# Kernel optimization log

Hardware: AMD Instinct MI355X
Metric: run time of the kernel (lower is better)

## Reference

```python
import jax, jax.numpy as jnp
import numpy as np


def _lstm_last(x, wih, whh, bih, bhh):
    """PyTorch-semantics LSTM over x [B, T, I]; returns last hidden state [B, H].
    Gate order in weights: i, f, g, o (PyTorch convention)."""
    B = x.shape[0]
    H = whh.shape[1]
    b = bih + bhh

    def step(carry, xt):
        h, c = carry
        g = xt @ wih.T + h @ whh.T + b  # [B, 4H]
        i, f, gg, o = jnp.split(g, 4, axis=-1)
        c = jax.nn.sigmoid(f) * c + jax.nn.sigmoid(i) * jnp.tanh(gg)
        h = jax.nn.sigmoid(o) * jnp.tanh(c)
        return (h, c), None

    h0 = jnp.zeros((B, H), x.dtype)
    (h, _), _ = jax.lax.scan(step, (h0, h0), jnp.swapaxes(x, 0, 1))
    return h


def setup_inputs() -> dict:
    key = jax.random.key(0)
    ks = jax.random.split(key, 16)
    B, N, T = 512, 32, 50
    s = 0.05
    return {
        "agent_traj": jax.random.normal(ks[0], (B, T, 2), jnp.float32),
        "neighbour_traj": jax.random.normal(ks[1], (B, N, T, 2), jnp.float32),
        "a_wih": jax.random.normal(ks[2], (256, 2), jnp.float32) * s,
        "a_whh": jax.random.normal(ks[3], (256, 64), jnp.float32) * s,
        "a_bih": jax.random.normal(ks[4], (256,), jnp.float32) * s,
        "a_bhh": jax.random.normal(ks[5], (256,), jnp.float32) * s,
        "n_wih": jax.random.normal(ks[6], (256, 2), jnp.float32) * s,
        "n_whh": jax.random.normal(ks[7], (256, 64), jnp.float32) * s,
        "n_bih": jax.random.normal(ks[8], (256,), jnp.float32) * s,
        "n_bhh": jax.random.normal(ks[9], (256,), jnp.float32) * s,
        "d_wih": jax.random.normal(ks[10], (512, 128), jnp.float32) * s,
        "d_whh": jax.random.normal(ks[11], (512, 128), jnp.float32) * s,
        "d_bih": jax.random.normal(ks[12], (512,), jnp.float32) * s,
        "d_bhh": jax.random.normal(ks[13], (512,), jnp.float32) * s,
        "e_w": jax.random.normal(ks[14], (2, 128), jnp.float32) * s,
        "e_b": jax.random.normal(ks[15], (2,), jnp.float32) * s,
    }


def reference(agent_traj, neighbour_traj, a_wih, a_whh, a_bih, a_bhh,
              n_wih, n_whh, n_bih, n_bhh, d_wih, d_whh, d_bih, d_bhh, e_w, e_b):
    B, N, T, _ = neighbour_traj.shape
    # agent encoder: last hidden state [B, 64]
    agent_emb = _lstm_last(agent_traj, a_wih, a_whh, a_bih, a_bhh)
    # neighbour encoder: batch all B*N ragged sequences as one LSTM call, then mean over neighbours
    nh = _lstm_last(neighbour_traj.reshape(B * N, T, 2), n_wih, n_whh, n_bih, n_bhh)
    neigh_emb = nh.reshape(B, N, 64).mean(axis=1)  # [B, 64]

    h0 = jnp.concatenate([agent_emb, neigh_emb], axis=1)  # [B, 128]
    c0 = jnp.zeros_like(h0)
    db = d_bih + d_bhh

    def dec_step(carry, _):
        h, c = carry
        # LSTMCell with input = h itself
        g = h @ d_wih.T + h @ d_whh.T + db  # [B, 512]
        i, f, gg, o = jnp.split(g, 4, axis=-1)
        c = jax.nn.sigmoid(f) * c + jax.nn.sigmoid(i) * jnp.tanh(gg)
        h = jax.nn.sigmoid(o) * jnp.tanh(c)
        pred = h @ e_w.T + e_b  # [B, 2]
        return (h, c), pred

    _, preds = jax.lax.scan(dec_step, (h0, c0), None, length=30)  # [30, B, 2]
    return jnp.swapaxes(preds, 0, 1)  # [B, 30, 2]
```

## Files before the change

### kernel.cpp

```cpp
#include <hip/hip_runtime.h>
#include <hip/hip_bf16.h>


typedef __attribute__((ext_vector_type(8))) short bf16x8;
typedef __attribute__((ext_vector_type(4))) float f32x4;
typedef unsigned int uint;
typedef unsigned short ushort_t;

#define LOG2E  1.4426950408889634f
#define LOG2E2 2.8853900817779268f

__device__ __forceinline__ float rcp_fast(float x) { return __builtin_amdgcn_rcpf(x); }
__device__ __forceinline__ float exp2_fast(float x) { return __builtin_amdgcn_exp2f(x); }
__device__ __forceinline__ float sigf(float x) { return rcp_fast(1.0f + __expf(-x)); }
__device__ __forceinline__ float tanh_fast(float x) {
    x = fminf(fmaxf(x, -15.0f), 15.0f);
    float e = __expf(2.0f * x);
    return (e - 1.0f) * rcp_fast(e + 1.0f);
}
__device__ __forceinline__ ushort_t bf_hi(float f) {
    union { float f; uint u; } v; v.f = f;
    return (ushort_t)(v.u >> 16);
}
__device__ __forceinline__ ushort_t bf_rtn(float f) {
    union { float f; uint u; } v; v.f = f;
    return (ushort_t)((v.u + 0x7FFFu + ((v.u >> 16) & 1u)) >> 16);
}
__device__ __forceinline__ float bf_f(ushort_t h) {
    union { float f; uint u; } v; v.u = ((uint)h) << 16;
    return v.f;
}

__device__ __forceinline__ float cell_update_p(float xi, float xf, float xg,
                                               float xo, float& c) {
    float pi = exp2_fast(-xi);
    float pf = exp2_fast(-xf);
    float po = exp2_fast(-xo);
    float pg = exp2_fast(fminf(xg, 120.0f));
    float f  = rcp_fast(1.0f + pf);
    float ig = (pg - 1.0f) * rcp_fast((1.0f + pi) * (pg + 1.0f));
    float cc = __builtin_fmaf(f, c, ig);
    c = cc;
    float e2 = exp2_fast(fminf(cc * LOG2E2, 120.0f));
    return (e2 - 1.0f) * rcp_fast((1.0f + po) * (e2 + 1.0f));
}

#define HS 36

__global__ __launch_bounds__(256, 4) void enc10_kernel(
    const float* __restrict__ ax, const float* __restrict__ nx,
    const float* __restrict__ a_wih, const float* __restrict__ a_whh,
    const float* __restrict__ a_bih, const float* __restrict__ a_bhh,
    const float* __restrict__ n_wih, const float* __restrict__ n_whh,
    const float* __restrict__ n_bih, const float* __restrict__ n_bhh,
    float* __restrict__ nh_out, float* __restrict__ ah_out)
{
    const int tid = threadIdx.x, blk = blockIdx.x;
    const bool agent = (blk >= 1024);
    const int seq0 = (agent ? (blk - 1024) : blk) * 16;
    const float* __restrict__ x   = agent ? ax : nx;
    const float* __restrict__ wih = agent ? a_wih : n_wih;
    const float* __restrict__ whh = agent ? a_whh : n_whh;
    const float* __restrict__ bih = agent ? a_bih : n_bih;
    const float* __restrict__ bhh = agent ? a_bhh : n_bhh;
    float* __restrict__ hout = agent ? ah_out : nh_out;

    const int lane = tid & 63, wv = tid >> 6;
    const int col = lane & 15, quad = lane >> 4;

    __shared__ __attribute__((aligned(16))) uint hb[2][16][HS];
    __shared__ __attribute__((aligned(16))) ushort_t xb[50][16][8];

    bf16x8 Aw[4][2];
    #pragma unroll
    for (int g = 0; g < 4; ++g) {
        const float sc = (g == 2) ? LOG2E2 : LOG2E;
        #pragma unroll
        for (int kt = 0; kt < 2; ++kt) {
            const float* p = whh + (size_t)(g * 64 + 16 * wv + col) * 64 + kt * 32 + quad * 8;
            float4 v0 = *(const float4*)p;
            float4 v1 = *(const float4*)(p + 4);
            float vv[8] = { v0.x, v0.y, v0.z, v0.w, v1.x, v1.y, v1.z, v1.w };
            bf16x8 h8;
            #pragma unroll
            for (int j = 0; j < 8; ++j) h8[j] = (short)bf_rtn(vv[j] * sc);
            Aw[g][kt] = h8;
        }
    }

    bf16x8 Ax[4];
    #pragma unroll
    for (int g = 0; g < 4; ++g) {
        const float sc = (g == 2) ? LOG2E2 : LOG2E;
        bf16x8 a;
        #pragma unroll
        for (int j = 0; j < 8; ++j) a[j] = 0;
        if (quad == 0) {
            const int row = g * 64 + 16 * wv + col;
            float w0 = wih[2 * row] * sc, w1 = wih[2 * row + 1] * sc;
            float b  = (bih[row] + bhh[row]) * sc;
            ushort_t w0h = bf_hi(w0), w1h = bf_hi(w1);
            ushort_t bh  = bf_hi(b);
            a[0] = (short)w0h;
            a[1] = (short)w1h;
            a[2] = (short)bf_hi(w0 - bf_f(w0h));
            a[3] = (short)bf_hi(w1 - bf_f(w1h));
            a[4] = (short)w0h;
            a[5] = (short)w1h;
            a[6] = (short)bh;
            a[7] = (short)bf_hi(b - bf_f(bh));
        }
        Ax[g] = a;
    }

    for (int idx = tid; idx < 50 * 16; idx += 256) {
        const int t = idx >> 4, s = idx & 15;
        const float* xp = x + (size_t)(seq0 + s) * 100 + 2 * t;
        float x0 = xp[0], x1 = xp[1];
        ushort_t h0 = bf_hi(x0), h1 = bf_hi(x1);
        ushort_t* e = &xb[t][s][0];
        e[0] = h0; e[1] = h1;
        e[2] = h0; e[3] = h1;
        e[4] = bf_hi(x0 - bf_f(h0));
        e[5] = bf_hi(x1 - bf_f(h1));
        e[6] = 0x3F80; e[7] = 0x3F80;
    }
    for (int i = tid; i < 16 * HS; i += 256) (&hb[0][0][0])[i] = 0u;
    __syncthreads();

    float c[4] = {0.f, 0.f, 0.f, 0.f};
    bf16x8 Bx = *(const bf16x8*)&xb[0][col][0];

    for (int t = 0; t < 50; ++t) {
        const int cur = t & 1, nxt = cur ^ 1;

        const f32x4 z4 = {0.f, 0.f, 0.f, 0.f};
        f32x4 acc[4];
        #pragma unroll
        for (int g = 0; g < 4; ++g)
            acc[g] = __builtin_amdgcn_mfma_f32_16x16x32_bf16(Ax[g], Bx, z4, 0, 0, 0);

        #pragma unroll
        for (int kt = 0; kt < 2; ++kt) {
            bf16x8 Bhi = *(const bf16x8*)&hb[cur][col][kt * 16 + quad * 4];
            #pragma unroll
            for (int g = 0; g < 4; ++g)
                acc[g] = __builtin_amdgcn_mfma_f32_16x16x32_bf16(Aw[g][kt], Bhi, acc[g], 0, 0, 0);
        }

        float hv[4];
        #pragma unroll
        for (int r = 0; r < 4; ++r)
            hv[r] = cell_update_p(acc[0][r], acc[1][r], acc[2][r], acc[3][r], c[r]);

        {
            __hip_bfloat162 p01 = __float22bfloat162_rn(make_float2(hv[0], hv[1]));
            __hip_bfloat162 p23 = __float22bfloat162_rn(make_float2(hv[2], hv[3]));
            uint2 hi2;
            union { __hip_bfloat162 b; uint u; } c0, c1;
            c0.b = p01; c1.b = p23;
            hi2.x = c0.u;
            hi2.y = c1.u;
            const int di = 8 * wv + 2 * quad;
            *(uint2*)&hb[nxt][col][di] = hi2;
        }
        if (t < 49) Bx = *(const bf16x8*)&xb[t + 1][col][0];
        if (t == 49) {
            #pragma unroll
            for (int r = 0; r < 4; ++r)
                hout[(size_t)(seq0 + col) * 64 + 16 * wv + 4 * quad + r] = hv[r];
        }
        __syncthreads();
    }
}

__global__ __launch_bounds__(512) void dec10_kernel(
    const float* __restrict__ ah, const float* __restrict__ nh,
    const float* __restrict__ d_wih, const float* __restrict__ d_whh,
    const float* __restrict__ d_bih, const float* __restrict__ d_bhh,
    const float* __restrict__ e_w, const float* __restrict__ e_b,
    float* __restrict__ out)
{
    const int tid = threadIdx.x;
    const int blk = blockIdx.x;

    const int u  = tid >> 2;
    const int tt = tid & 3;
    const int r  = tt * 128 + u;

    float w[128];
    #pragma unroll
    for (int k = 0; k < 128; k += 4) {
        float4 aa = *(const float4*)(d_wih + r * 128 + k);
        float4 bb = *(const float4*)(d_whh + r * 128 + k);
        w[k]   = aa.x + bb.x;
        w[k+1] = aa.y + bb.y;
        w[k+2] = aa.z + bb.z;
        w[k+3] = aa.w + bb.w;
    }
    const float bias = d_bih[r] + d_bhh[r];

    __shared__ float hs[2][128];
    __shared__ float cs[2][128];
    __shared__ float gs[2][512];
    __shared__ float ews[2][128];
    __shared__ float ebs[2];

    if (tid < 256) {
        const int s = tid >> 7, j = tid & 127;
        const int gseq = blk * 2 + s;
        float v;
        if (j < 64) {
            v = ah[(size_t)gseq * 64 + j];
        } else {
            float acc = 0.0f;
            for (int n = 0; n < 32; ++n)
                acc += nh[(size_t)(gseq * 32 + n) * 64 + (j - 64)];
            v = acc * (1.0f / 32.0f);
        }
        hs[s][j] = v;
        cs[s][j] = 0.0f;
        ews[s][j] = e_w[tid];
    }
    if (tid < 2) ebs[tid] = e_b[tid];
    __syncthreads();

    for (int t = 0; t < 30; ++t) {
        #pragma unroll
        for (int s = 0; s < 2; ++s) {
            const float4* hp = (const float4*)(&hs[s][0]);
            float a0 = 0.f, a1 = 0.f, a2 = 0.f, a3 = 0.f;
            #pragma unroll
            for (int k = 0; k < 32; ++k) {
                float4 h4 = hp[k];
                a0 = __builtin_fmaf(w[4*k+0], h4.x, a0);
                a1 = __builtin_fmaf(w[4*k+1], h4.y, a1);
                a2 = __builtin_fmaf(w[4*k+2], h4.z, a2);
                a3 = __builtin_fmaf(w[4*k+3], h4.w, a3);
            }
            gs[s][tid] = bias + ((a0 + a1) + (a2 + a3));
        }
        __syncthreads();
        if (tid < 256) {
            const int s = tid >> 7, j = tid & 127;
            float4 g4 = *(const float4*)(&gs[s][4 * j]);
            float ig = sigf(g4.x), fg = sigf(g4.y);
            float gg = tanh_fast(g4.z), og = sigf(g4.w);
            float c = fg * cs[s][j] + ig * gg;
            cs[s][j] = c;
            hs[s][j] = og * tanh_fast(c);
        }
        __syncthreads();
        {
            const int wv = tid >> 6, l = tid & 63;
            if (wv < 4) {
                const int s = wv >> 1, o = wv & 1;
                float p = hs[s][l] * ews[o][l] + hs[s][64 + l] * ews[o][64 + l];
                #pragma unroll
                for (int off = 32; off > 0; off >>= 1) p += __shfl_down(p, off);
                if (l == 0) out[((size_t)(blk * 2 + s) * 30 + t) * 2 + o] = p + ebs[o];
            }
        }
    }
}

extern "C" void kernel_launch(void* const* d_in, const int* in_sizes, int n_in,
                              void* d_out, int out_size, void* d_ws, size_t ws_size,
                              hipStream_t stream)
{
    const float* agent_traj = (const float*)d_in[0];
    const float* neigh_traj = (const float*)d_in[1];
    const float* a_wih = (const float*)d_in[2];
    const float* a_whh = (const float*)d_in[3];
    const float* a_bih = (const float*)d_in[4];
    const float* a_bhh = (const float*)d_in[5];
    const float* n_wih = (const float*)d_in[6];
    const float* n_whh = (const float*)d_in[7];
    const float* n_bih = (const float*)d_in[8];
    const float* n_bhh = (const float*)d_in[9];
    const float* d_wih = (const float*)d_in[10];
    const float* d_whh = (const float*)d_in[11];
    const float* d_bih = (const float*)d_in[12];
    const float* d_bhh = (const float*)d_in[13];
    const float* e_w   = (const float*)d_in[14];
    const float* e_b   = (const float*)d_in[15];
    float* out = (float*)d_out;

    float* nh_ws = (float*)d_ws;
    float* ah_ws = nh_ws + 16384 * 64;

    enc10_kernel<<<dim3(1024 + 32), dim3(256), 0, stream>>>(
        agent_traj, neigh_traj,
        a_wih, a_whh, a_bih, a_bhh,
        n_wih, n_whh, n_bih, n_bhh,
        nh_ws, ah_ws);

    dec10_kernel<<<dim3(256), dim3(512), 0, stream>>>(
        ah_ws, nh_ws, d_wih, d_whh, d_bih, d_bhh, e_w, e_b, out);
}
```

Measured before the change: 247.4 us.

## Run each encoder block as a single wavefront computing all 64 hidden units

```diff
diff --git a/kernel.cpp b/kernel.cpp
--- a/kernel.cpp
+++ b/kernel.cpp
@@ -47,7 +47,7 @@
 
 #define HS 36
 
-__global__ __launch_bounds__(256, 4) void enc10_kernel(
+__global__ __launch_bounds__(64, 1) void enc11_kernel(
     const float* __restrict__ ax, const float* __restrict__ nx,
     const float* __restrict__ a_wih, const float* __restrict__ a_whh,
     const float* __restrict__ a_bih, const float* __restrict__ a_bhh,
@@ -65,55 +65,60 @@
     const float* __restrict__ bhh = agent ? a_bhh : n_bhh;
     float* __restrict__ hout = agent ? ah_out : nh_out;
 
-    const int lane = tid & 63, wv = tid >> 6;
-    const int col = lane & 15, quad = lane >> 4;
+    const int c = tid & 15, q = tid >> 4;
 
     __shared__ __attribute__((aligned(16))) uint hb[2][16][HS];
     __shared__ __attribute__((aligned(16))) ushort_t xb[50][16][8];
 
-    bf16x8 Aw[4][2];
+    bf16x8 Aw[4][4][2];
     #pragma unroll
     for (int g = 0; g < 4; ++g) {
         const float sc = (g == 2) ? LOG2E2 : LOG2E;
         #pragma unroll
-        for (int kt = 0; kt < 2; ++kt) {
-            const float* p = whh + (size_t)(g * 64 + 16 * wv + col) * 64 + kt * 32 + quad * 8;
-            float4 v0 = *(const float4*)p;
-            float4 v1 = *(const float4*)(p + 4);
-            float vv[8] = { v0.x, v0.y, v0.z, v0.w, v1.x, v1.y, v1.z, v1.w };
-            bf16x8 h8;
-            #pragma unroll
-            for (int j = 0; j < 8; ++j) h8[j] = (short)bf_rtn(vv[j] * sc);
-            Aw[g][kt] = h8;
-        }
-    }
-
-    bf16x8 Ax[4];
+        for (int ug = 0; ug < 4; ++ug) {
+            #pragma unroll
+            for (int kt = 0; kt < 2; ++kt) {
+                const float* p = whh + (size_t)(g * 64 + 16 * ug + c) * 64 + kt * 32 + q * 8;
+                float4 v0 = *(const float4*)p;
+                float4 v1 = *(const float4*)(p + 4);
+                float vv[8] = { v0.x, v0.y, v0.z, v0.w, v1.x, v1.y, v1.z, v1.w };
+                bf16x8 h8;
+                #pragma unroll
+                for (int j = 0; j < 8; ++j) h8[j] = (short)bf_rtn(vv[j] * sc);
+                Aw[g][ug][kt] = h8;
+            }
+        }
+    }
+
+    bf16x8 Axx[4][4];
     #pragma unroll
     for (int g = 0; g < 4; ++g) {
         const float sc = (g == 2) ? LOG2E2 : LOG2E;
-        bf16x8 a;
-        #pragma unroll
-        for (int j = 0; j < 8; ++j) a[j] = 0;
-        if (quad == 0) {
-            const int row = g * 64 + 16 * wv + col;
-            float w0 = wih[2 * row] * sc, w1 = wih[2 * row + 1] * sc;
-            float b  = (bih[row] + bhh[row]) * sc;
-            ushort_t w0h = bf_hi(w0), w1h = bf_hi(w1);
-            ushort_t bh  = bf_hi(b);
-            a[0] = (short)w0h;
-            a[1] = (short)w1h;
-            a[2] = (short)bf_hi(w0 - bf_f(w0h));
-            a[3] = (short)bf_hi(w1 - bf_f(w1h));
-            a[4] = (short)w0h;
-            a[5] = (short)w1h;
-            a[6] = (short)bh;
-            a[7] = (short)bf_hi(b - bf_f(bh));
-        }
-        Ax[g] = a;
-    }
-
-    for (int idx = tid; idx < 50 * 16; idx += 256) {
+        #pragma unroll
+        for (int ug = 0; ug < 4; ++ug) {
+            bf16x8 a;
+            #pragma unroll
+            for (int j = 0; j < 8; ++j) a[j] = 0;
+            if (q == 0) {
+                const int row = g * 64 + 16 * ug + c;
+                float w0 = wih[2 * row] * sc, w1 = wih[2 * row + 1] * sc;
+                float b  = (bih[row] + bhh[row]) * sc;
+                ushort_t w0h = bf_hi(w0), w1h = bf_hi(w1);
+                ushort_t bh  = bf_hi(b);
+                a[0] = (short)w0h;
+                a[1] = (short)w1h;
+                a[2] = (short)bf_hi(w0 - bf_f(w0h));
+                a[3] = (short)bf_hi(w1 - bf_f(w1h));
+                a[4] = (short)w0h;
+                a[5] = (short)w1h;
+                a[6] = (short)bh;
+                a[7] = (short)bf_hi(b - bf_f(bh));
+            }
+            Axx[g][ug] = a;
+        }
+    }
+
+    for (int idx = tid; idx < 50 * 16; idx += 64) {
         const int t = idx >> 4, s = idx & 15;
         const float* xp = x + (size_t)(seq0 + s) * 100 + 2 * t;
         float x0 = xp[0], x1 = xp[1];
@@ -125,56 +130,61 @@
         e[5] = bf_hi(x1 - bf_f(h1));
         e[6] = 0x3F80; e[7] = 0x3F80;
     }
-    for (int i = tid; i < 16 * HS; i += 256) (&hb[0][0][0])[i] = 0u;
+    for (int i = tid; i < 16 * HS; i += 64) (&hb[0][0][0])[i] = 0u;
     __syncthreads();
 
-    float c[4] = {0.f, 0.f, 0.f, 0.f};
-    bf16x8 Bx = *(const bf16x8*)&xb[0][col][0];
+    float cst[4][4];
+    #pragma unroll
+    for (int ug = 0; ug < 4; ++ug)
+        #pragma unroll
+        for (int r = 0; r < 4; ++r) cst[ug][r] = 0.0f;
+
+    bf16x8 Bx = *(const bf16x8*)&xb[0][c][0];
 
     for (int t = 0; t < 50; ++t) {
         const int cur = t & 1, nxt = cur ^ 1;
 
+        bf16x8 B0 = *(const bf16x8*)&hb[cur][c][q * 4];
+        bf16x8 B1 = *(const bf16x8*)&hb[cur][c][16 + q * 4];
+
         const f32x4 z4 = {0.f, 0.f, 0.f, 0.f};
-        f32x4 acc[4];
-        #pragma unroll
-        for (int g = 0; g < 4; ++g)
-            acc[g] = __builtin_amdgcn_mfma_f32_16x16x32_bf16(Ax[g], Bx, z4, 0, 0, 0);
-
-        #pragma unroll
-        for (int kt = 0; kt < 2; ++kt) {
-            bf16x8 Bhi = *(const bf16x8*)&hb[cur][col][kt * 16 + quad * 4];
+        #pragma unroll
+        for (int ug = 0; ug < 4; ++ug) {
+            f32x4 acc[4];
             #pragma unroll
             for (int g = 0; g < 4; ++g)
-                acc[g] = __builtin_amdgcn_mfma_f32_16x16x32_bf16(Aw[g][kt], Bhi, acc[g], 0, 0, 0);
-        }
-
-        float hv[4];
-        #pragma unroll
-        for (int r = 0; r < 4; ++r)
-            hv[r] = cell_update_p(acc[0][r], acc[1][r], acc[2][r], acc[3][r], c[r]);
-
-        {
-            __hip_bfloat162 p01 = __float22bfloat162_rn(make_float2(hv[0], hv[1]));
-            __hip_bfloat162 p23 = __float22bfloat162_rn(make_float2(hv[2], hv[3]));
-            uint2 hi2;
-            union { __hip_bfloat162 b; uint u; } c0, c1;
-            c0.b = p01; c1.b = p23;
-            hi2.x = c0.u;
-            hi2.y = c1.u;
-            const int di = 8 * wv + 2 * quad;
-            *(uint2*)&hb[nxt][col][di] = hi2;
-        }
-        if (t < 49) Bx = *(const bf16x8*)&xb[t + 1][col][0];
-        if (t == 49) {
+                acc[g] = __builtin_amdgcn_mfma_f32_16x16x32_bf16(Axx[g][ug], Bx, z4, 0, 0, 0);
+            #pragma unroll
+            for (int g = 0; g < 4; ++g)
+                acc[g] = __builtin_amdgcn_mfma_f32_16x16x32_bf16(Aw[g][ug][0], B0, acc[g], 0, 0, 0);
+            #pragma unroll
+            for (int g = 0; g < 4; ++g)
+                acc[g] = __builtin_amdgcn_mfma_f32_16x16x32_bf16(Aw[g][ug][1], B1, acc[g], 0, 0, 0);
+
+            float hv[4];
             #pragma unroll
             for (int r = 0; r < 4; ++r)
-                hout[(size_t)(seq0 + col) * 64 + 16 * wv + 4 * quad + r] = hv[r];
-        }
+                hv[r] = cell_update_p(acc[0][r], acc[1][r], acc[2][r], acc[3][r], cst[ug][r]);
+
+            {
+                __hip_bfloat162 p01 = __float22bfloat162_rn(make_float2(hv[0], hv[1]));
+                __hip_bfloat162 p23 = __float22bfloat162_rn(make_float2(hv[2], hv[3]));
+                union { __hip_bfloat162 b; uint u; } c0, c1;
+                c0.b = p01; c1.b = p23;
+                uint2 w; w.x = c0.u; w.y = c1.u;
+                *(uint2*)&hb[nxt][c][8 * ug + 2 * q] = w;
+            }
+            if (t == 49) {
+                float4 o4 = make_float4(hv[0], hv[1], hv[2], hv[3]);
+                *(float4*)(hout + (size_t)(seq0 + c) * 64 + 16 * ug + 4 * q) = o4;
+            }
+        }
+        if (t < 49) Bx = *(const bf16x8*)&xb[t + 1][c][0];
         __syncthreads();
     }
 }
 
-__global__ __launch_bounds__(512) void dec10_kernel(
+__global__ __launch_bounds__(512) void dec11_kernel(
     const float* __restrict__ ah, const float* __restrict__ nh,
     const float* __restrict__ d_wih, const float* __restrict__ d_whh,
     const float* __restrict__ d_bih, const float* __restrict__ d_bhh,
@@ -246,9 +256,9 @@
             float4 g4 = *(const float4*)(&gs[s][4 * j]);
             float ig = sigf(g4.x), fg = sigf(g4.y);
             float gg = tanh_fast(g4.z), og = sigf(g4.w);
-            float c = fg * cs[s][j] + ig * gg;
-            cs[s][j] = c;
-            hs[s][j] = og * tanh_fast(c);
+            float cc = fg * cs[s][j] + ig * gg;
+            cs[s][j] = cc;
+            hs[s][j] = og * tanh_fast(cc);
         }
         __syncthreads();
         {
@@ -289,12 +299,12 @@
     float* nh_ws = (float*)d_ws;
     float* ah_ws = nh_ws + 16384 * 64;
 
-    enc10_kernel<<<dim3(1024 + 32), dim3(256), 0, stream>>>(
+    enc11_kernel<<<dim3(1024 + 32), dim3(64), 0, stream>>>(
         agent_traj, neigh_traj,
         a_wih, a_whh, a_bih, a_bhh,
         n_wih, n_whh, n_bih, n_bhh,
         nh_ws, ah_ws);
 
-    dec10_kernel<<<dim3(256), dim3(512), 0, stream>>>(
+    dec11_kernel<<<dim3(256), dim3(512), 0, stream>>>(
         ah_ws, nh_ws, d_wih, d_whh, d_bih, d_bhh, e_w, e_b, out);
 }
```

Result: slower. 328.7 us (+32.9%).
